# Kernel tuning notes

Hardware: AMD Instinct MI355X
Metric: run time of the kernel (lower is better)

## Reference

```python
import jax, jax.numpy as jnp
import numpy as np

V, E, H, B, T = 50000, 256, 512, 64, 2048

def setup_inputs() -> dict:
    key = jax.random.key(0)
    ks = jax.random.split(key, 16)
    s = lambda *shp: 1.0 / np.sqrt(shp[-1])
    emb = jax.random.normal(ks[0], (V, E), dtype=jnp.float32) * 0.02
    emb = emb.at[0].set(0.0)  # padding_idx=0 row zeroed
    inp = {
        "input_token": jax.random.randint(ks[1], (B,), 0, V),
        "hidden": jax.random.normal(ks[2], (1, B, H), dtype=jnp.float32),
        "cell": jax.random.normal(ks[3], (1, B, H), dtype=jnp.float32),
        "encoder_outputs": jax.random.normal(ks[4], (B, T, H), dtype=jnp.float32),
        "emb": emb,
        "W_enc": jax.random.normal(ks[5], (H, H), dtype=jnp.float32) * s(H, H),
        "W_dec": jax.random.normal(ks[6], (H, H), dtype=jnp.float32) * s(H, H),
        "v_attn": jax.random.normal(ks[7], (H,), dtype=jnp.float32) * s(H),
        "W_ih": jax.random.normal(ks[8], (4 * H, E + H), dtype=jnp.float32) * s(4 * H, E + H),
        "W_hh": jax.random.normal(ks[9], (4 * H, H), dtype=jnp.float32) * s(4 * H, H),
        "b_ih": jax.random.normal(ks[10], (4 * H,), dtype=jnp.float32) * 0.01,
        "b_hh": jax.random.normal(ks[11], (4 * H,), dtype=jnp.float32) * 0.01,
        "W_out": jax.random.normal(ks[12], (V, 2 * H), dtype=jnp.float32) * s(V, 2 * H),
        "b_out": jnp.zeros((V,), dtype=jnp.float32),
    }
    return inp

def reference(input_token, hidden, cell, encoder_outputs, emb, W_enc, W_dec,
              v_attn, W_ih, W_hh, b_ih, b_hh, W_out, b_out):
    h = hidden[0]  # (B,H)
    c = cell[0]    # (B,H)
    # embedding lookup (dropout is identity at eval)
    embedded = emb[input_token]  # (B,E)
    # Bahdanau attention
    energy = jnp.tanh(encoder_outputs @ W_enc.T + (h @ W_dec.T)[:, None, :])  # (B,T,H)
    scores = energy @ v_attn  # (B,T)
    attn = jax.nn.softmax(scores, axis=1)
    context = jnp.einsum('bt,bth->bh', attn, encoder_outputs)  # (B,H)
    # single-step LSTM (PyTorch gate order: i, f, g, o)
    x = jnp.concatenate([embedded, context], axis=1)  # (B,E+H)
    gates = x @ W_ih.T + b_ih + h @ W_hh.T + b_hh  # (B,4H)
    i_g, f_g, g_g, o_g = jnp.split(gates, 4, axis=1)
    i_g = jax.nn.sigmoid(i_g)
    f_g = jax.nn.sigmoid(f_g)
    g_g = jnp.tanh(g_g)
    o_g = jax.nn.sigmoid(o_g)
    c_new = f_g * c + i_g * g_g
    h_new = o_g * jnp.tanh(c_new)
    # output projection
    logits = jnp.concatenate([h_new, context], axis=1) @ W_out.T + b_out  # (B,V)
    return logits, h_new[None], c_new[None], attn
```

## Files before the change

kernel.cpp:

```cpp
#include <hip/hip_runtime.h>

#define V_SZ 50000
#define E_SZ 256
#define H_SZ 512
#define B_SZ 64
#define T_SZ 2048

#define H_OFF    (B_SZ * V_SZ)
#define C_OFF    (H_OFF + B_SZ * H_SZ)
#define ATTN_OFF (C_OFF + B_SZ * H_SZ)

#define WS_X    0
#define WS_HW   (WS_X + B_SZ * 768)
#define WS_SC   (WS_HW + B_SZ * H_SZ)
#define WS_CTXP (WS_SC + B_SZ * T_SZ)
#define WS_X2   (WS_CTXP + 16 * B_SZ * H_SZ)
#define WS_GP   (WS_X2 + B_SZ * 1024)
#define WS_WB   (WS_GP + 8 * B_SZ * 2048)

typedef __attribute__((ext_vector_type(8))) short bf16x8;
typedef __attribute__((ext_vector_type(4))) float floatx4;

__device__ __forceinline__ float fast_tanh(float x) {
    return 1.f - 2.f / (__expf(2.f * x) + 1.f);
}
__device__ __forceinline__ float fast_sigmoid(float x) {
    return 1.f / (1.f + __expf(-x));
}
__device__ __forceinline__ unsigned short f2bf(float f) {
    union { float f; unsigned u; } v; v.f = f;
    unsigned r = v.u + 0x7FFFu + ((v.u >> 16) & 1u);
    return (unsigned short)(r >> 16);
}

__global__ void k0_wenc_bf16(const float* __restrict__ W_enc, float* __restrict__ ws) {
    unsigned short* Wb = (unsigned short*)(ws + WS_WB);
    const int i = (blockIdx.x * 256 + threadIdx.x) * 8;
    float4 a = *(const float4*)(W_enc + i);
    float4 b = *(const float4*)(W_enc + i + 4);
    ushort4 lo = {f2bf(a.x), f2bf(a.y), f2bf(a.z), f2bf(a.w)};
    ushort4 hi = {f2bf(b.x), f2bf(b.y), f2bf(b.z), f2bf(b.w)};
    *(ushort4*)(Wb + i) = lo;
    *(ushort4*)(Wb + i + 4) = hi;
}

__global__ void k1_embed_hw(const int* __restrict__ tok, const float* __restrict__ hidden,
                            const float* __restrict__ emb, const float* __restrict__ W_dec,
                            float* __restrict__ ws) {
    const int b = blockIdx.x, tid = threadIdx.x;
    __shared__ __align__(16) float sh[512];
    sh[tid]       = hidden[b * 512 + tid];
    sh[tid + 256] = hidden[b * 512 + tid + 256];
    const int t = tok[b];
    ws[WS_X + b * 768 + tid] = emb[t * 256 + tid];
    __syncthreads();
    for (int jr = tid; jr < 512; jr += 256) {
        const float* w = W_dec + jr * 512;
        float acc = 0.f;
        #pragma unroll 8
        for (int k = 0; k < 512; k += 4) {
            float4 wv = *(const float4*)(w + k);
            float4 hv = *(const float4*)(sh + k);
            acc += wv.x * hv.x + wv.y * hv.y + wv.z * hv.z + wv.w * hv.w;
        }
        ws[WS_HW + b * 512 + jr] = acc;
    }
}

__global__ __launch_bounds__(256, 2)
void k2_scores(const float* __restrict__ enc, const float* __restrict__ v_attn,
               float* __restrict__ ws) {
    __shared__ __align__(16) unsigned short As[64 * 40];
    __shared__ __align__(16) unsigned short Bs[512 * 40];
    __shared__ float sp[4][64];
    const unsigned short* Wb = (const unsigned short*)(ws + WS_WB);
    const int tid = threadIdx.x;
    const int lane = tid & 63, wv = tid >> 6;
    const int lane15 = lane & 15, quad = lane >> 4;
    const int t0 = blockIdx.x * 64, b = blockIdx.y;
    const int wn = wv * 128;

    floatx4 acc[4][8];
    #pragma unroll
    for (int mt = 0; mt < 4; mt++)
        #pragma unroll
        for (int nt = 0; nt < 8; nt++) acc[mt][nt] = (floatx4){0.f, 0.f, 0.f, 0.f};

    for (int kt = 0; kt < 512; kt += 32) {
        __syncthreads();
        #pragma unroll
        for (int q = 0; q < 2; q++) {
            int f = tid + 256 * q;
            int row = f >> 3, kq = f & 7;
            float4 v = *(const float4*)(enc + (size_t)(b * 2048 + t0 + row) * 512 + kt + kq * 4);
            ushort4 h = {f2bf(v.x), f2bf(v.y), f2bf(v.z), f2bf(v.w)};
            *(ushort4*)(As + row * 40 + kq * 4) = h;
        }
        #pragma unroll
        for (int q = 0; q < 8; q++) {
            int f = tid + 256 * q;
            int row = f >> 2, c = f & 3;
            uint4 w = *(const uint4*)(Wb + row * 512 + kt + c * 8);
            *(uint4*)(Bs + row * 40 + c * 8) = w;
        }
        __syncthreads();

        bf16x8 af[4];
        #pragma unroll
        for (int mt = 0; mt < 4; mt++)
            af[mt] = *(const bf16x8*)(As + (mt * 16 + lane15) * 40 + quad * 8);
        #pragma unroll
        for (int nt = 0; nt < 8; nt++) {
            bf16x8 bf = *(const bf16x8*)(Bs + (wn + nt * 16 + lane15) * 40 + quad * 8);
            #pragma unroll
            for (int mt = 0; mt < 4; mt++)
                acc[mt][nt] = __builtin_amdgcn_mfma_f32_16x16x32_bf16(af[mt], bf, acc[mt][nt], 0, 0, 0);
        }
    }

    float vj[8], hwj[8];
    #pragma unroll
    for (int nt = 0; nt < 8; nt++) {
        int jg = wn + nt * 16 + lane15;
        vj[nt] = v_attn[jg];
        hwj[nt] = ws[WS_HW + b * 512 + jg];
    }
    #pragma unroll
    for (int mt = 0; mt < 4; mt++) {
        #pragma unroll
        for (int reg = 0; reg < 4; reg++) {
            int row = mt * 16 + quad * 4 + reg;
            float s = 0.f;
            #pragma unroll
            for (int nt = 0; nt < 8; nt++)
                s += vj[nt] * fast_tanh(acc[mt][nt][reg] + hwj[nt]);
            #pragma unroll
            for (int off = 8; off; off >>= 1) s += __shfl_xor(s, off);
            if (lane15 == 0) sp[wv][row] = s;
        }
    }
    __syncthreads();
    if (tid < 64)
        ws[WS_SC + b * 2048 + t0 + tid] = sp[0][tid] + sp[1][tid] + sp[2][tid] + sp[3][tid];
}

__global__ void k3_softmax(const float* __restrict__ ws, float* __restrict__ out) {
    const int b = blockIdx.x, tid = threadIdx.x;
    const float* s0 = ws + WS_SC + b * 2048;
    float sv[8];
    float m = -1e30f;
    #pragma unroll
    for (int i = 0; i < 8; i++) {
        int t = tid + 256 * i;
        sv[i] = s0[t];
        m = fmaxf(m, sv[i]);
    }
    #pragma unroll
    for (int o = 32; o; o >>= 1) m = fmaxf(m, __shfl_xor(m, o, 64));
    __shared__ float red[4], red2[4];
    if ((tid & 63) == 0) red[tid >> 6] = m;
    __syncthreads();
    m = fmaxf(fmaxf(red[0], red[1]), fmaxf(red[2], red[3]));
    float sum = 0.f;
    #pragma unroll
    for (int i = 0; i < 8; i++) { sv[i] = __expf(sv[i] - m); sum += sv[i]; }
    #pragma unroll
    for (int o = 32; o; o >>= 1) sum += __shfl_xor(sum, o, 64);
    if ((tid & 63) == 0) red2[tid >> 6] = sum;
    __syncthreads();
    sum = red2[0] + red2[1] + red2[2] + red2[3];
    const float inv = 1.f / sum;
    #pragma unroll
    for (int i = 0; i < 8; i++) {
        int t = tid + 256 * i;
        out[ATTN_OFF + b * 2048 + t] = sv[i] * inv;
    }
}

__global__ void k4_ctx(const float* __restrict__ enc, const float* __restrict__ attn_out,
                       float* __restrict__ ws) {
    const int ts = blockIdx.x, b = blockIdx.y, tid = threadIdx.x;
    const float* attn = attn_out + ATTN_OFF + b * 2048 + ts * 128;
    const float* ep = enc + (size_t)(b * 2048 + ts * 128) * 512 + tid * 2;
    float2 acc = {0.f, 0.f};
    #pragma unroll 4
    for (int tt = 0; tt < 128; tt++) {
        float a = attn[tt];
        float2 e = *(const float2*)(ep + (size_t)tt * 512);
        acc.x += a * e.x;
        acc.y += a * e.y;
    }
    *(float2*)(ws + WS_CTXP + (ts * 64 + b) * 512 + tid * 2) = acc;
}

__global__ void k4b_ctx_reduce(float* __restrict__ ws) {
    const int idx = blockIdx.x * 256 + threadIdx.x;
    const int b = idx >> 9, h = idx & 511;
    float s = 0.f;
    #pragma unroll
    for (int c = 0; c < 16; c++) s += ws[WS_CTXP + c * (B_SZ * 512) + b * 512 + h];
    ws[WS_X + b * 768 + 256 + h] = s;
    ws[WS_X2 + b * 1024 + 512 + h] = s;
}

__global__ __launch_bounds__(256, 2)
void k5_gates(const float* __restrict__ hidden, const float* __restrict__ W_ih,
              const float* __restrict__ W_hh, float* __restrict__ ws) {
    __shared__ __align__(16) float Wg[128 * 12];
    __shared__ __align__(16) float Zs[64 * 8];
    const int tid = threadIdx.x;
    const int jb = tid & 31, tg = tid >> 5;
    const int g0 = blockIdx.x * 128;
    const int kc = blockIdx.y;
    const int kbase = kc * 160;
    const float* xp = ws + WS_X;

    float acc[8][4];
    #pragma unroll
    for (int r = 0; r < 8; r++)
        #pragma unroll
        for (int j = 0; j < 4; j++) acc[r][j] = 0.f;

    for (int kt0 = 0; kt0 < 160; kt0 += 8) {
        const int kt = kbase + kt0;
        __syncthreads();
        {
            int row = tid >> 1, kq = tid & 1;
            int k = kt + kq * 4;
            const float* src = (k < 768) ? (W_ih + (g0 + row) * 768 + k)
                                         : (W_hh + (g0 + row) * 512 + (k - 768));
            *(float4*)(Wg + row * 12 + kq * 4) = *(const float4*)src;
        }
        if (tid < 128) {
            int row = tid >> 1, kq = tid & 1;
            int k = kt + kq * 4;
            const float* src = (k < 768) ? (xp + row * 768 + k)
                                         : (hidden + row * 512 + (k - 768));
            *(float4*)(Zs + row * 8 + kq * 4) = *(const float4*)src;
        }
        __syncthreads();

        float er[8][8];
        #pragma unroll
        for (int r = 0; r < 8; r++) {
            float4 a = *(const float4*)(Zs + (tg * 8 + r) * 8);
            float4 c = *(const float4*)(Zs + (tg * 8 + r) * 8 + 4);
            er[r][0] = a.x; er[r][1] = a.y; er[r][2] = a.z; er[r][3] = a.w;
            er[r][4] = c.x; er[r][5] = c.y; er[r][6] = c.z; er[r][7] = c.w;
        }
        #pragma unroll
        for (int jj = 0; jj < 4; jj++) {
            const float* wr = Wg + (jb + 32 * jj) * 12;
            float4 w0 = *(const float4*)(wr);
            float4 w1 = *(const float4*)(wr + 4);
            float w[8] = {w0.x, w0.y, w0.z, w0.w, w1.x, w1.y, w1.z, w1.w};
            #pragma unroll
            for (int r = 0; r < 8; r++)
                #pragma unroll
                for (int k = 0; k < 8; k++) acc[r][jj] += er[r][k] * w[k];
        }
    }
    #pragma unroll
    for (int jj = 0; jj < 4; jj++)
        #pragma unroll
        for (int r = 0; r < 8; r++)
            ws[WS_GP + kc * (B_SZ * 2048) + (tg * 8 + r) * 2048 + g0 + jb + 32 * jj] = acc[r][jj];
}

__global__ void k5b_lstm(const float* __restrict__ cell, const float* __restrict__ b_ih,
                         const float* __restrict__ b_hh, float* __restrict__ ws,
                         float* __restrict__ out) {
    const int e = blockIdx.x * 256 + threadIdx.x;
    const int b = e >> 9, hh = e & 511;
    float g4[4];
    #pragma unroll
    for (int q = 0; q < 4; q++) {
        float s = b_ih[q * 512 + hh] + b_hh[q * 512 + hh];
        #pragma unroll
        for (int c = 0; c < 8; c++)
            s += ws[WS_GP + c * (B_SZ * 2048) + b * 2048 + q * 512 + hh];
        g4[q] = s;
    }
    const float ig = fast_sigmoid(g4[0]);
    const float fg = fast_sigmoid(g4[1]);
    const float gg = fast_tanh(g4[2]);
    const float og = fast_sigmoid(g4[3]);
    const float c_old = cell[b * 512 + hh];
    const float c_new = fg * c_old + ig * gg;
    const float h_new = og * fast_tanh(c_new);
    out[H_OFF + b * 512 + hh] = h_new;
    out[C_OFF + b * 512 + hh] = c_new;
    ws[WS_X2 + b * 1024 + hh] = h_new;
}

__global__ __launch_bounds__(256, 2)
void k6_logits(const float* __restrict__ W_out, const float* __restrict__ b_out,
               const float* __restrict__ ws, float* __restrict__ out) {
    __shared__ __align__(16) unsigned short Xs[64 * 40];
    __shared__ __align__(16) unsigned short Ws2[256 * 40];
    const float* x2 = ws + WS_X2;
    const int tid = threadIdx.x;
    const int lane = tid & 63, wv = tid >> 6;
    const int lane15 = lane & 15, quad = lane >> 4;
    const int v0 = blockIdx.x * 256;
    const int wn = wv * 64;

    floatx4 acc[4][4];
    #pragma unroll
    for (int mt = 0; mt < 4; mt++)
        #pragma unroll
        for (int nt = 0; nt < 4; nt++) acc[mt][nt] = (floatx4){0.f, 0.f, 0.f, 0.f};

    for (int kt = 0; kt < 1024; kt += 32) {
        __syncthreads();
        #pragma unroll
        for (int q = 0; q < 2; q++) {
            int f = tid + 256 * q;
            int row = f >> 3, kq = f & 7;
            float4 v = *(const float4*)(x2 + row * 1024 + kt + kq * 4);
            ushort4 h = {f2bf(v.x), f2bf(v.y), f2bf(v.z), f2bf(v.w)};
            *(ushort4*)(Xs + row * 40 + kq * 4) = h;
        }
        #pragma unroll
        for (int q = 0; q < 8; q++) {
            int f = tid + 256 * q;
            int row = f >> 3, kq = f & 7;
            int v = v0 + row; if (v > V_SZ - 1) v = V_SZ - 1;
            float4 w = *(const float4*)(W_out + (size_t)v * 1024 + kt + kq * 4);
            ushort4 h = {f2bf(w.x), f2bf(w.y), f2bf(w.z), f2bf(w.w)};
            *(ushort4*)(Ws2 + row * 40 + kq * 4) = h;
        }
        __syncthreads();

        bf16x8 af[4];
        #pragma unroll
        for (int mt = 0; mt < 4; mt++)
            af[mt] = *(const bf16x8*)(Xs + (mt * 16 + lane15) * 40 + quad * 8);
        #pragma unroll
        for (int nt = 0; nt < 4; nt++) {
            bf16x8 bf = *(const bf16x8*)(Ws2 + (wn + nt * 16 + lane15) * 40 + quad * 8);
            #pragma unroll
            for (int mt = 0; mt < 4; mt++)
                acc[mt][nt] = __builtin_amdgcn_mfma_f32_16x16x32_bf16(af[mt], bf, acc[mt][nt], 0, 0, 0);
        }
    }

    #pragma unroll
    for (int nt = 0; nt < 4; nt++) {
        const int v = v0 + wn + nt * 16 + lane15;
        if (v < V_SZ) {
            const float bo = b_out[v];
            #pragma unroll
            for (int mt = 0; mt < 4; mt++)
                #pragma unroll
                for (int reg = 0; reg < 4; reg++) {
                    const int br = mt * 16 + quad * 4 + reg;
                    out[br * V_SZ + v] = acc[mt][nt][reg] + bo;
                }
        }
    }
}

extern "C" void kernel_launch(void* const* d_in, const int* in_sizes, int n_in,
                              void* d_out, int out_size, void* d_ws, size_t ws_size,
                              hipStream_t stream) {
    (void)in_sizes; (void)n_in; (void)out_size; (void)ws_size;
    const int*   tok    = (const int*)d_in[0];
    const float* hidden = (const float*)d_in[1];
    const float* cell   = (const float*)d_in[2];
    const float* enc    = (const float*)d_in[3];
    const float* emb    = (const float*)d_in[4];
    const float* W_enc  = (const float*)d_in[5];
    const float* W_dec  = (const float*)d_in[6];
    const float* v_attn = (const float*)d_in[7];
    const float* W_ih   = (const float*)d_in[8];
    const float* W_hh   = (const float*)d_in[9];
    const float* b_ih   = (const float*)d_in[10];
    const float* b_hh   = (const float*)d_in[11];
    const float* W_out  = (const float*)d_in[12];
    const float* b_out  = (const float*)d_in[13];
    float* out = (float*)d_out;
    float* ws  = (float*)d_ws;

    k0_wenc_bf16<<<dim3(128), dim3(256), 0, stream>>>(W_enc, ws);
    k1_embed_hw<<<dim3(64), dim3(256), 0, stream>>>(tok, hidden, emb, W_dec, ws);
    k2_scores<<<dim3(32, 64), dim3(256), 0, stream>>>(enc, v_attn, ws);
    k3_softmax<<<dim3(64), dim3(256), 0, stream>>>(ws, out);
    k4_ctx<<<dim3(16, 64), dim3(256), 0, stream>>>(enc, out, ws);
    k4b_ctx_reduce<<<dim3(128), dim3(256), 0, stream>>>(ws);
    k5_gates<<<dim3(16, 8), dim3(256), 0, stream>>>(hidden, W_ih, W_hh, ws);
    k5b_lstm<<<dim3(128), dim3(256), 0, stream>>>(cell, b_ih, b_hh, ws, out);
    k6_logits<<<dim3(196), dim3(256), 0, stream>>>(W_out, b_out, ws, out);
}
```

Baseline: 828.0 us.

## Double-buffer W_enc tiles via async global-to-LDS loads, load A directly to registers

Pre-swizzles the bf16 W_enc copy into per-k-slice contiguous tiles so the scores kernel can stream each 32-wide K slice into LDS with global_load_lds async copies, double-buffered across iterations. The encoder-output A operand no longer goes through LDS: each lane loads its fp32 fragment directly into registers, prefetched one step ahead, and converts it with packed bf16 conversion instructions. This removes one barrier per iteration and the LDS round-trip for A. LDS use rises to two 32KB buffers, which may limit occupancy.

```diff
diff --git a/kernel.cpp b/kernel.cpp
--- a/kernel.cpp
+++ b/kernel.cpp
@@ -33,15 +33,35 @@
     return (unsigned short)(r >> 16);
 }
 
+__device__ __forceinline__ bf16x8 cvt8(float4 a, float4 b) {
+    union { unsigned u[4]; bf16x8 v; } r;
+    asm("v_cvt_pk_bf16_f32 %0, %1, %2" : "=v"(r.u[0]) : "v"(a.x), "v"(a.y));
+    asm("v_cvt_pk_bf16_f32 %0, %1, %2" : "=v"(r.u[1]) : "v"(a.z), "v"(a.w));
+    asm("v_cvt_pk_bf16_f32 %0, %1, %2" : "=v"(r.u[2]) : "v"(b.x), "v"(b.y));
+    asm("v_cvt_pk_bf16_f32 %0, %1, %2" : "=v"(r.u[3]) : "v"(b.z), "v"(b.w));
+    return r.v;
+}
+
+__device__ __forceinline__ void async_copy16(void* lds, const void* g) {
+    __builtin_amdgcn_global_load_lds(
+        (const __attribute__((address_space(1))) unsigned int*)g,
+        (__attribute__((address_space(3))) unsigned int*)lds, 16, 0, 0);
+}
+
 __global__ void k0_wenc_bf16(const float* __restrict__ W_enc, float* __restrict__ ws) {
     unsigned short* Wb = (unsigned short*)(ws + WS_WB);
-    const int i = (blockIdx.x * 256 + threadIdx.x) * 8;
-    float4 a = *(const float4*)(W_enc + i);
-    float4 b = *(const float4*)(W_enc + i + 4);
+    const int id = blockIdx.x * 256 + threadIdx.x;
+    const int j = id >> 6, kc = id & 63;
+    const int k = kc * 8;
+    float4 a = *(const float4*)(W_enc + j * 512 + k);
+    float4 b4 = *(const float4*)(W_enc + j * 512 + k + 4);
     ushort4 lo = {f2bf(a.x), f2bf(a.y), f2bf(a.z), f2bf(a.w)};
-    ushort4 hi = {f2bf(b.x), f2bf(b.y), f2bf(b.z), f2bf(b.w)};
-    *(ushort4*)(Wb + i) = lo;
-    *(ushort4*)(Wb + i + 4) = hi;
+    ushort4 hi = {f2bf(b4.x), f2bf(b4.y), f2bf(b4.z), f2bf(b4.w)};
+    const int s = kc >> 2, q = kc & 3;
+    const int u = 4 * j + ((q + j) & 3);
+    unsigned short* dst = Wb + s * 16384 + u * 8;
+    *(ushort4*)(dst) = lo;
+    *(ushort4*)(dst + 4) = hi;
 }
 
 __global__ void k1_embed_hw(const int* __restrict__ tok, const float* __restrict__ hidden,
@@ -70,8 +90,7 @@
 __global__ __launch_bounds__(256, 2)
 void k2_scores(const float* __restrict__ enc, const float* __restrict__ v_attn,
                float* __restrict__ ws) {
-    __shared__ __align__(16) unsigned short As[64 * 40];
-    __shared__ __align__(16) unsigned short Bs[512 * 40];
+    __shared__ __align__(16) unsigned short Bs[2][16384];
     __shared__ float sp[4][64];
     const unsigned short* Wb = (const unsigned short*)(ws + WS_WB);
     const int tid = threadIdx.x;
@@ -80,42 +99,60 @@
     const int t0 = blockIdx.x * 64, b = blockIdx.y;
     const int wn = wv * 128;
 
+    const float* aBase = enc + ((size_t)(b * 2048 + t0 + lane15)) * 512 + quad * 8;
+
+    const int j0 = wn + lane15;
+    const int rdBase = 64 * j0 + 16 * ((quad + j0) & 3);
+
     floatx4 acc[4][8];
     #pragma unroll
     for (int mt = 0; mt < 4; mt++)
         #pragma unroll
         for (int nt = 0; nt < 8; nt++) acc[mt][nt] = (floatx4){0.f, 0.f, 0.f, 0.f};
 
-    for (int kt = 0; kt < 512; kt += 32) {
+    float4 aF[4][2];
+    {
+        const char* gs = (const char*)Wb;
+        #pragma unroll
+        for (int q8 = 0; q8 < 8; ++q8)
+            async_copy16((char*)&Bs[0][0] + q8 * 4096 + tid * 16, gs + q8 * 4096 + tid * 16);
+        #pragma unroll
+        for (int mt = 0; mt < 4; ++mt) {
+            aF[mt][0] = *(const float4*)(aBase + mt * 8192);
+            aF[mt][1] = *(const float4*)(aBase + mt * 8192 + 4);
+        }
+    }
+    __syncthreads();
+
+    for (int t = 0; t < 16; ++t) {
+        const int cur = t & 1;
+        if (t < 15) {
+            char* nb = (char*)&Bs[cur ^ 1][0];
+            const char* gs = (const char*)(Wb + (t + 1) * 16384);
+            #pragma unroll
+            for (int q8 = 0; q8 < 8; ++q8)
+                async_copy16(nb + q8 * 4096 + tid * 16, gs + q8 * 4096 + tid * 16);
+        }
+        bf16x8 af[4];
+        #pragma unroll
+        for (int mt = 0; mt < 4; ++mt) af[mt] = cvt8(aF[mt][0], aF[mt][1]);
+        if (t < 15) {
+            const float* ab = aBase + (t + 1) * 32;
+            #pragma unroll
+            for (int mt = 0; mt < 4; ++mt) {
+                aF[mt][0] = *(const float4*)(ab + mt * 8192);
+                aF[mt][1] = *(const float4*)(ab + mt * 8192 + 4);
+            }
+        }
+        const char* bs = (const char*)&Bs[cur][0];
+        #pragma unroll
+        for (int nt = 0; nt < 8; ++nt) {
+            bf16x8 bfr = *(const bf16x8*)(bs + rdBase + nt * 1024);
+            #pragma unroll
+            for (int mt = 0; mt < 4; ++mt)
+                acc[mt][nt] = __builtin_amdgcn_mfma_f32_16x16x32_bf16(af[mt], bfr, acc[mt][nt], 0, 0, 0);
+        }
         __syncthreads();
-        #pragma unroll
-        for (int q = 0; q < 2; q++) {
-            int f = tid + 256 * q;
-            int row = f >> 3, kq = f & 7;
-            float4 v = *(const float4*)(enc + (size_t)(b * 2048 + t0 + row) * 512 + kt + kq * 4);
-            ushort4 h = {f2bf(v.x), f2bf(v.y), f2bf(v.z), f2bf(v.w)};
-            *(ushort4*)(As + row * 40 + kq * 4) = h;
-        }
-        #pragma unroll
-        for (int q = 0; q < 8; q++) {
-            int f = tid + 256 * q;
-            int row = f >> 2, c = f & 3;
-            uint4 w = *(const uint4*)(Wb + row * 512 + kt + c * 8);
-            *(uint4*)(Bs + row * 40 + c * 8) = w;
-        }
-        __syncthreads();
-
-        bf16x8 af[4];
-        #pragma unroll
-        for (int mt = 0; mt < 4; mt++)
-            af[mt] = *(const bf16x8*)(As + (mt * 16 + lane15) * 40 + quad * 8);
-        #pragma unroll
-        for (int nt = 0; nt < 8; nt++) {
-            bf16x8 bf = *(const bf16x8*)(Bs + (wn + nt * 16 + lane15) * 40 + quad * 8);
-            #pragma unroll
-            for (int mt = 0; mt < 4; mt++)
-                acc[mt][nt] = __builtin_amdgcn_mfma_f32_16x16x32_bf16(af[mt], bf, acc[mt][nt], 0, 0, 0);
-        }
     }
 
     float vj[8], hwj[8];
```

Measured after the change: 880.3 us. +6.3%, slower.
